# Optimization experiments

Hardware: AMD Instinct MI355X
Metric: run time of the kernel (lower is better)

## Reference

```python
import jax, jax.numpy as jnp
import numpy as np

N, M, D = 6144, 6144, 128
EPS = 1e-12


def setup_inputs() -> dict:
    key = jax.random.key(0)
    k1, k2 = jax.random.split(key)
    desc1 = jax.random.normal(k1, (N, D), dtype=jnp.float32)
    desc2 = jax.random.normal(k2, (M, D), dtype=jnp.float32)
    # DISK descriptors are unit-normalized; distances in the docstring are in [0, 2]
    desc1 = desc1 / jnp.linalg.norm(desc1, axis=-1, keepdims=True)
    desc2 = desc2 / jnp.linalg.norm(desc2, axis=-1, keepdims=True)
    inverse_T = jnp.asarray(15.0, dtype=jnp.float32)  # learned scalar nn.Parameter
    return {"desc1": desc1, "desc2": desc2, "inverse_T": inverse_T}


def reference(desc1, desc2, inverse_T):
    # pairwise Euclidean distance matrix [N, M]
    sq1 = jnp.sum(desc1 * desc1, axis=-1)            # [N]
    sq2 = jnp.sum(desc2 * desc2, axis=-1)            # [M]
    inner = desc1 @ desc2.T                           # [N, M] GEMM, D=128
    d2 = sq1[:, None] + sq2[None, :] - 2.0 * inner
    distances = jnp.sqrt(jnp.maximum(d2, 0.0) + EPS)  # [N, M]

    affinity = -inverse_T * distances                 # scaled logits

    # Categorical(logits=affinity).logits  == log_softmax over rows
    # Categorical(logits=affinity.T).logits.T == log_softmax over columns
    logp_I = jax.nn.log_softmax(affinity, axis=1)     # row distribution [N, M]
    logp_T = jax.nn.log_softmax(affinity, axis=0)     # col distribution [N, M]

    dense_logp = logp_I + logp_T                      # dual-softmax log prob
    dense_p = jnp.exp(logp_I) * jnp.exp(logp_T)       # dual-softmax prob

    # mle(): argmax matches with cycle-consistency check
    maxes_I = jnp.argmax(affinity, axis=1)            # [N] best col per row
    maxes_T = jnp.argmax(affinity, axis=0)            # [M] best row per col
    idx = jnp.arange(N)
    cycle_consistent = maxes_T[maxes_I] == idx        # [N] bool mask
    # Original returns stack([right[paired_left], paired_left]) over the
    # consistent subset; here we keep fixed shape [2, N] + the mask
    # (matches[:, i] valid iff cycle_consistent[i]).
    matches = jnp.stack([idx, maxes_I], axis=0)       # [2, N] int

    return dense_logp, dense_p, matches, cycle_consistent
```

## Files before the change

kernel.cpp:

```cpp
#include <hip/hip_runtime.h>
#include <hip/hip_bf16.h>
#include <stdint.h>

#define NROWS 6144
#define MCOLS 6144
#define DDIM  128
#define EPSQ  1e-12f
#define NTC   48

typedef unsigned long long ull;
typedef __attribute__((ext_vector_type(8))) short short8;
typedef __attribute__((ext_vector_type(4))) float floatx4;

__device__ __forceinline__ ull makeKey(float v, int idx) {
    unsigned u = __float_as_uint(v);
    u = (u & 0x80000000u) ? ~u : (u | 0x80000000u);
    return ((ull)u << 32) | (ull)(0xFFFFFFFFu - (unsigned)idx);
}
__device__ __forceinline__ int decodeKeyIdx(ull k) {
    return (int)(0xFFFFFFFFu - (unsigned)(k & 0xFFFFFFFFull));
}
__device__ __forceinline__ unsigned short f2bf(float f) {
    unsigned u = __float_as_uint(f);
    u += 0x7fffu + ((u >> 16) & 1);
    return (unsigned short)(u >> 16);
}

#define DPPF(x, ctrl) __uint_as_float(__builtin_amdgcn_update_dpp( \
    0, (int)__float_as_uint(x), (ctrl), 0xF, 0xF, false))
#define DPPI(x, ctrl) __builtin_amdgcn_update_dpp(0, (x), (ctrl), 0xF, 0xF, false)
#define ROR8 0x128
#define ROR4 0x124
#define ROR2 0x122
#define ROR1 0x121

#define GLOAD16(g, l) \
  __builtin_amdgcn_global_load_lds((const __attribute__((address_space(1))) unsigned int*)(g), \
                                   (__attribute__((address_space(3))) unsigned int*)(l), 16, 0, 0)

__device__ __forceinline__ void tileCoord(int& rowBase, int& colBase) {
    int id  = blockIdx.x;
    int wid = (id & 7) * (NTC * NTC / 8) + (id >> 3);
    rowBase = (wid / NTC) * 128;
    colBase = (wid % NTC) * 128;
}

__global__ __launch_bounds__(256) void convert_kernel(
    const float* __restrict__ d1, const float* __restrict__ d2,
    unsigned short* __restrict__ s1, unsigned short* __restrict__ s2,
    float* __restrict__ sq1, float* __restrict__ sq2,
    unsigned* __restrict__ zero_region)
{
    int tid = blockIdx.x * 256 + threadIdx.x;
    if (tid < 36864) zero_region[tid] = 0u;

    int row = tid >> 4;
    int sub = tid & 15;
    if (row >= NROWS + MCOLS) return;
    bool isA = row < NROWS;
    int r = isA ? row : row - NROWS;
    const float* src = (isA ? d1 : d2) + (size_t)r * DDIM + sub * 8;
    unsigned short* dst = (isA ? s1 : s2) + (size_t)r * 256;

    float4 v0 = *(const float4*)(src);
    float4 v1 = *(const float4*)(src + 4);
    float vs[8] = {v0.x, v0.y, v0.z, v0.w, v1.x, v1.y, v1.z, v1.w};

    float s = 0.f;
    #pragma unroll
    for (int j = 0; j < 8; ++j) s += vs[j] * vs[j];
    #pragma unroll
    for (int m = 1; m < 16; m <<= 1) s += __shfl_xor(s, m, 64);
    if (sub == 0) { if (isA) sq1[r] = s; else sq2[r] = s; }

    short8 hi, lo;
    #pragma unroll
    for (int j = 0; j < 8; ++j) {
        unsigned short h = f2bf(vs[j]);
        hi[j] = (short)h;
        lo[j] = (short)f2bf(vs[j] - __uint_as_float((unsigned)h << 16));
    }
    int e  = sub * 8;
    int c  = e >> 6;
    int pe = (e & 63) ^ ((r & 7) << 3);
    *(short8*)(dst + c * 128 + pe)      = hi;
    *(short8*)(dst + c * 128 + 64 + pe) = lo;
}

__device__ __forceinline__ void stageBuf(
    const unsigned short* __restrict__ gpanel, unsigned short* buf,
    int c, int h, int t)
{
    #pragma unroll
    for (int it = 0; it < 2; ++it) {
        int li = t * 8 + it * 4096;
        int r  = li >> 6, e = li & 63;
        int gi = r * 256 + c * 128 + h * 64 + e;
        GLOAD16(gpanel + gi, &buf[li]);
    }
}

__device__ __forceinline__ void computeSplit(
    const unsigned short* Ab_, const unsigned short* Bb_,
    int lane, int wr, int wc, floatx4 acc[4][2])
{
    const int l15 = lane & 15;
    const int q16 = (lane >> 4) * 16;
    const int sw  = (l15 & 7) << 4;
    const char* Ab = (const char*)Ab_;
    const char* Bb = (const char*)Bb_;
    #pragma unroll
    for (int ks = 0; ks < 2; ++ks) {
        const int kk = (ks * 64 + q16) ^ sw;
        short8 af[4], bf[2];
        #pragma unroll
        for (int mi = 0; mi < 4; ++mi)
            af[mi] = *(const short8*)(Ab + (wr * 64 + mi * 16 + l15) * 128 + kk);
        #pragma unroll
        for (int ni = 0; ni < 2; ++ni)
            bf[ni] = *(const short8*)(Bb + (wc * 32 + ni * 16 + l15) * 128 + kk);
        #pragma unroll
        for (int mi = 0; mi < 4; ++mi)
            #pragma unroll
            for (int ni = 0; ni < 2; ++ni)
                acc[mi][ni] = __builtin_amdgcn_mfma_f32_16x16x32_bf16(
                    bf[ni], af[mi], acc[mi][ni], 0, 0, 0);
    }
}

__device__ __forceinline__ void computeSplitAB2(
    const unsigned short* Ab_, const unsigned short* B0_, const unsigned short* B1_,
    int lane, int wr, int wc, floatx4 acc[4][2])
{
    const int l15 = lane & 15;
    const int q16 = (lane >> 4) * 16;
    const int sw  = (l15 & 7) << 4;
    const char* Ab = (const char*)Ab_;
    const char* B0 = (const char*)B0_;
    const char* B1 = (const char*)B1_;
    #pragma unroll
    for (int ks = 0; ks < 2; ++ks) {
        const int kk = (ks * 64 + q16) ^ sw;
        short8 af[4], bf0[2], bf1[2];
        #pragma unroll
        for (int mi = 0; mi < 4; ++mi)
            af[mi] = *(const short8*)(Ab + (wr * 64 + mi * 16 + l15) * 128 + kk);
        #pragma unroll
        for (int ni = 0; ni < 2; ++ni) {
            bf0[ni] = *(const short8*)(B0 + (wc * 32 + ni * 16 + l15) * 128 + kk);
            bf1[ni] = *(const short8*)(B1 + (wc * 32 + ni * 16 + l15) * 128 + kk);
        }
        #pragma unroll
        for (int mi = 0; mi < 4; ++mi)
            #pragma unroll
            for (int ni = 0; ni < 2; ++ni)
                acc[mi][ni] = __builtin_amdgcn_mfma_f32_16x16x32_bf16(
                    bf0[ni], af[mi], acc[mi][ni], 0, 0, 0);
        #pragma unroll
        for (int mi = 0; mi < 4; ++mi)
            #pragma unroll
            for (int ni = 0; ni < 2; ++ni)
                acc[mi][ni] = __builtin_amdgcn_mfma_f32_16x16x32_bf16(
                    bf1[ni], af[mi], acc[mi][ni], 0, 0, 0);
    }
}

__global__ __launch_bounds__(512, 4) void gemm_reduce_kernel(
    const unsigned short* __restrict__ s1, const unsigned short* __restrict__ s2,
    const float* __restrict__ invT,
    const float* __restrict__ sq1, const float* __restrict__ sq2,
    float* __restrict__ rowsum, float* __restrict__ colsum,
    ull* __restrict__ rowkey, ull* __restrict__ colkey)
{
    __shared__ unsigned short A0[8192], A1[8192], B0[8192], B1[8192];
    __shared__ float lRowS[128], lColS[128];
    __shared__ ull   lRowK[128], lColK[128];

    const int t = threadIdx.x;
    const int lane = t & 63;
    const int wave = t >> 6;
    const int wr = wave >> 2, wc = wave & 3;
    int rowBase, colBase;
    tileCoord(rowBase, colBase);
    const unsigned short* gA = s1 + (size_t)rowBase * 256;
    const unsigned short* gB = s2 + (size_t)colBase * 256;

    if (t < 128) { lRowS[t] = 0.f; lColS[t] = 0.f; lRowK[t] = 0ull; lColK[t] = 0ull; }

    floatx4 acc[4][2] = {};
    stageBuf(gA, A0, 0, 0, t); stageBuf(gB, B0, 0, 0, t); stageBuf(gB, B1, 0, 1, t);
    __syncthreads();
    stageBuf(gA, A1, 0, 1, t);
    computeSplitAB2(A0, B0, B1, lane, wr, wc, acc);
    __syncthreads();
    stageBuf(gA, A0, 1, 0, t); stageBuf(gB, B1, 1, 0, t);
    computeSplit(A1, B0, lane, wr, wc, acc);
    __syncthreads();
    stageBuf(gA, A1, 1, 1, t); stageBuf(gB, B0, 1, 1, t);
    computeSplit(A0, B1, lane, wr, wc, acc);
    __syncthreads();
    computeSplit(A0, B0, lane, wr, wc, acc);
    computeSplit(A1, B1, lane, wr, wc, acc);

    const int l15 = lane & 15;
    const int q   = lane >> 4;
    const float iT = *invT;
    float s1r[4];
    #pragma unroll
    for (int mi = 0; mi < 4; ++mi)
        s1r[mi] = sq1[rowBase + wr * 64 + mi * 16 + l15] + EPSQ;
    const int colLoc0 = wc * 32 + q * 4;
    float4 s2v[2];
    #pragma unroll
    for (int ni = 0; ni < 2; ++ni)
        s2v[ni] = *(const float4*)(sq2 + colBase + colLoc0 + ni * 16);

    float rs[4], rv[4]; int rj[4];
    float cs[2][4], cv[2][4]; int ci[2][4];
    #pragma unroll
    for (int ni = 0; ni < 2; ++ni)
        #pragma unroll
        for (int r = 0; r < 4; ++r) { cs[ni][r] = 0.f; cv[ni][r] = -1e30f; ci[ni][r] = 0; }

    #pragma unroll
    for (int mi = 0; mi < 4; ++mi) {
        const int gi = rowBase + wr * 64 + mi * 16 + l15;
        rs[mi] = 0.f; rv[mi] = -1e30f; rj[mi] = 0;
        #pragma unroll
        for (int ni = 0; ni < 2; ++ni) {
            #pragma unroll
            for (int r = 0; r < 4; ++r) {
                float sv2 = (r == 0) ? s2v[ni].x : (r == 1) ? s2v[ni].y
                          : (r == 2) ? s2v[ni].z : s2v[ni].w;
                float dd = s1r[mi] + sv2 - 2.0f * acc[mi][ni][r];
                float v = -iT * __builtin_amdgcn_sqrtf(fmaxf(dd, EPSQ));
                float e = __expf(v);
                rs[mi] += e;
                if (v > rv[mi]) { rv[mi] = v; rj[mi] = colBase + colLoc0 + ni * 16 + r; }
                cs[ni][r] += e;
                if (v > cv[ni][r]) { cv[ni][r] = v; ci[ni][r] = gi; }
            }
        }
    }

    #pragma unroll
    for (int mi = 0; mi < 4; ++mi) {
        float s = rs[mi];
        s += __shfl_xor(s, 16, 64); s += __shfl_xor(s, 32, 64);
        float v = rv[mi];
        v = fmaxf(v, __shfl_xor(v, 16, 64)); v = fmaxf(v, __shfl_xor(v, 32, 64));
        int cand = (rv[mi] == v) ? rj[mi] : 0x7FFFFFFF;
        cand = min(cand, __shfl_xor(cand, 16, 64));
        cand = min(cand, __shfl_xor(cand, 32, 64));
        if (lane < 16) {
            int idx = wr * 64 + mi * 16 + l15;
            atomicAdd(&lRowS[idx], s);
            atomicMax(&lRowK[idx], makeKey(v, cand));
        }
    }

    #pragma unroll
    for (int ni = 0; ni < 2; ++ni)
        #pragma unroll
        for (int r = 0; r < 4; ++r) {
            float s = cs[ni][r];
            s += DPPF(s, ROR8); s += DPPF(s, ROR4); s += DPPF(s, ROR2); s += DPPF(s, ROR1);
            float v = cv[ni][r];
            v = fmaxf(v, DPPF(v, ROR8)); v = fmaxf(v, DPPF(v, ROR4));
            v = fmaxf(v, DPPF(v, ROR2)); v = fmaxf(v, DPPF(v, ROR1));
            int cand = (cv[ni][r] == v) ? ci[ni][r] : 0x7FFFFFFF;
            cand = min(cand, DPPI(cand, ROR8)); cand = min(cand, DPPI(cand, ROR4));
            cand = min(cand, DPPI(cand, ROR2)); cand = min(cand, DPPI(cand, ROR1));
            if (l15 == 0) {
                int idx = colLoc0 + ni * 16 + r;
                atomicAdd(&lColS[idx], s);
                atomicMax(&lColK[idx], makeKey(v, cand));
            }
        }
    __syncthreads();

    if (t < 128) {
        atomicAdd(&rowsum[rowBase + t], lRowS[t]);
        atomicMax(&rowkey[rowBase + t], lRowK[t]);
    } else if (t < 256) {
        int j = t - 128;
        atomicAdd(&colsum[colBase + j], lColS[j]);
        atomicMax(&colkey[colBase + j], lColK[j]);
    }
}

#define VSTRIDE 132
__global__ __launch_bounds__(512, 4) void gemm_write_kernel(
    const unsigned short* __restrict__ s1, const unsigned short* __restrict__ s2,
    const float* __restrict__ invT,
    const float* __restrict__ sq1, const float* __restrict__ sq2,
    const float* __restrict__ rowsum, const float* __restrict__ colsum,
    const ull* __restrict__ rowkey, const ull* __restrict__ colkey,
    float* __restrict__ logp_out, float* __restrict__ p_out,
    float* __restrict__ out_matches, float* __restrict__ out_cyc)
{
    __shared__ char SMEM[128 * VSTRIDE * 4];
    unsigned short* A0 = (unsigned short*)(SMEM);
    unsigned short* A1 = (unsigned short*)(SMEM + 16384);
    unsigned short* B0 = (unsigned short*)(SMEM + 32768);
    unsigned short* B1 = (unsigned short*)(SMEM + 49152);
    float* V = (float*)SMEM;

    const int t = threadIdx.x;
    const int lane = t & 63;
    const int wave = t >> 6;
    const int wr = wave >> 2, wc = wave & 3;
    int rowBase, colBase;
    tileCoord(rowBase, colBase);
    const unsigned short* gA = s1 + (size_t)rowBase * 256;
    const unsigned short* gB = s2 + (size_t)colBase * 256;

    if (colBase == 0 && t < 128) {
        int i = rowBase + t;
        int mi = decodeKeyIdx(rowkey[i]);
        out_matches[i]         = (float)i;
        out_matches[NROWS + i] = (float)mi;
        out_cyc[i] = (decodeKeyIdx(colkey[mi]) == i) ? 1.0f : 0.0f;
    }

    floatx4 acc[4][2] = {};
    stageBuf(gA, A0, 0, 0, t); stageBuf(gB, B0, 0, 0, t);
    __syncthreads();
    stageBuf(gA, A1, 0, 1, t); stageBuf(gB, B1, 1, 0, t);
    computeSplit(A0, B0, lane, wr, wc, acc);
    __syncthreads();
    stageBuf(gA, A0, 1, 0, t);
    computeSplit(A1, B0, lane, wr, wc, acc);
    __syncthreads();
    stageBuf(gA, A1, 1, 1, t);
    computeSplit(A0, B1, lane, wr, wc, acc);
    __syncthreads();
    computeSplit(A1, B1, lane, wr, wc, acc);

    const int l15 = lane & 15;
    const int q   = lane >> 4;
    const float iT = *invT;
    float s1r[4];
    #pragma unroll
    for (int mi = 0; mi < 4; ++mi)
        s1r[mi] = sq1[rowBase + wr * 64 + mi * 16 + l15] + EPSQ;
    const int colLoc0 = wc * 32 + q * 4;
    float4 s2v[2];
    #pragma unroll
    for (int ni = 0; ni < 2; ++ni)
        s2v[ni] = *(const float4*)(sq2 + colBase + colLoc0 + ni * 16);

    __syncthreads();
    #pragma unroll
    for (int mi = 0; mi < 4; ++mi) {
        const int lrow = wr * 64 + mi * 16 + l15;
        #pragma unroll
        for (int ni = 0; ni < 2; ++ni) {
            floatx4 vv;
            #pragma unroll
            for (int r = 0; r < 4; ++r) {
                float sv2 = (r == 0) ? s2v[ni].x : (r == 1) ? s2v[ni].y
                          : (r == 2) ? s2v[ni].z : s2v[ni].w;
                float dd = s1r[mi] + sv2 - 2.0f * acc[mi][ni][r];
                vv[r] = -iT * __builtin_amdgcn_sqrtf(fmaxf(dd, EPSQ));
            }
            *(floatx4*)(V + lrow * VSTRIDE + colLoc0 + ni * 16) = vv;
        }
    }
    __syncthreads();

    const int rsub = lane >> 4;
    const int csub = (lane & 15) * 4;
    #pragma unroll
    for (int g = 0; g < 4; ++g) {
        const int lrow = wave * 16 + g * 4 + rsub;
        const int grow = rowBase + lrow;
        const float rl = logf(rowsum[grow]);
        #pragma unroll
        for (int h = 0; h < 2; ++h) {
            const int lcol = h * 64 + csub;
            float4 csum = *(const float4*)(colsum + colBase + lcol);
            float4 cl;
            cl.x = logf(csum.x); cl.y = logf(csum.y);
            cl.z = logf(csum.z); cl.w = logf(csum.w);
            float4 v4 = *(const float4*)(V + lrow * VSTRIDE + lcol);
            floatx4 ov, pv;
            ov[0] = (v4.x - rl) + (v4.x - cl.x); pv[0] = __expf(ov[0]);
            ov[1] = (v4.y - rl) + (v4.y - cl.y); pv[1] = __expf(ov[1]);
            ov[2] = (v4.z - rl) + (v4.z - cl.z); pv[2] = __expf(ov[2]);
            ov[3] = (v4.w - rl) + (v4.w - cl.w); pv[3] = __expf(ov[3]);
            size_t off = (size_t)grow * MCOLS + colBase + lcol;
            __builtin_nontemporal_store(ov, (floatx4*)(logp_out + off));
            __builtin_nontemporal_store(pv, (floatx4*)(p_out + off));
        }
    }
}

extern "C" void kernel_launch(void* const* d_in, const int* in_sizes, int n_in,
                              void* d_out, int out_size, void* d_ws, size_t ws_size,
                              hipStream_t stream) {
    const float* d1   = (const float*)d_in[0];
    const float* d2   = (const float*)d_in[1];
    const float* invT = (const float*)d_in[2];

    float* out     = (float*)d_out;
    float* logp    = out;
    float* pout    = out + (size_t)NROWS * MCOLS;
    float* matches = out + 2ull * NROWS * MCOLS;
    float* cyc     = matches + 2 * NROWS;

    char* ws = (char*)d_ws;
    float* rowsum = (float*)(ws + 0);
    float* colsum = (float*)(ws + 24576);
    ull*   rowkey = (ull*)(ws + 49152);
    ull*   colkey = (ull*)(ws + 98304);
    float* sq1    = (float*)(ws + 147456);
    float* sq2    = (float*)(ws + 172032);
    unsigned short* s1 = (unsigned short*)(ws + 270336);
    unsigned short* s2 = (unsigned short*)(ws + 270336 + 3145728);

    convert_kernel<<<(NROWS + MCOLS) * 16 / 256, 256, 0, stream>>>(
        d1, d2, s1, s2, sq1, sq2, (unsigned*)ws);

    gemm_reduce_kernel<<<NTC * NTC, 512, 0, stream>>>(
        s1, s2, invT, sq1, sq2, rowsum, colsum, rowkey, colkey);

    gemm_write_kernel<<<NTC * NTC, 512, 0, stream>>>(
        s1, s2, invT, sq1, sq2, rowsum, colsum, rowkey, colkey,
        logp, pout, matches, cyc);
}
```

Before: 127.9 us.

## Restructure split-bf16 GEMM staging into two K-chunks with fewer barriers

```diff
diff --git a/kernel.cpp b/kernel.cpp
--- a/kernel.cpp
+++ b/kernel.cpp
@@ -100,68 +100,88 @@
     }
 }
 
-__device__ __forceinline__ void computeSplit(
-    const unsigned short* Ab_, const unsigned short* Bb_,
+__device__ __forceinline__ void computeChunk3(
+    const unsigned short* Ah_, const unsigned short* Al_,
+    const unsigned short* Bh_, const unsigned short* Bl_,
     int lane, int wr, int wc, floatx4 acc[4][2])
 {
     const int l15 = lane & 15;
     const int q16 = (lane >> 4) * 16;
     const int sw  = (l15 & 7) << 4;
-    const char* Ab = (const char*)Ab_;
-    const char* Bb = (const char*)Bb_;
+    const char* Ah = (const char*)Ah_;
+    const char* Al = (const char*)Al_;
+    const char* Bh = (const char*)Bh_;
+    const char* Bl = (const char*)Bl_;
     #pragma unroll
     for (int ks = 0; ks < 2; ++ks) {
         const int kk = (ks * 64 + q16) ^ sw;
-        short8 af[4], bf[2];
-        #pragma unroll
-        for (int mi = 0; mi < 4; ++mi)
-            af[mi] = *(const short8*)(Ab + (wr * 64 + mi * 16 + l15) * 128 + kk);
-        #pragma unroll
-        for (int ni = 0; ni < 2; ++ni)
-            bf[ni] = *(const short8*)(Bb + (wc * 32 + ni * 16 + l15) * 128 + kk);
+        short8 afh[4], afl[4], bfh[2], bfl[2];
+        #pragma unroll
+        for (int mi = 0; mi < 4; ++mi) {
+            afh[mi] = *(const short8*)(Ah + (wr * 64 + mi * 16 + l15) * 128 + kk);
+            afl[mi] = *(const short8*)(Al + (wr * 64 + mi * 16 + l15) * 128 + kk);
+        }
+        #pragma unroll
+        for (int ni = 0; ni < 2; ++ni) {
+            bfh[ni] = *(const short8*)(Bh + (wc * 32 + ni * 16 + l15) * 128 + kk);
+            bfl[ni] = *(const short8*)(Bl + (wc * 32 + ni * 16 + l15) * 128 + kk);
+        }
         #pragma unroll
         for (int mi = 0; mi < 4; ++mi)
             #pragma unroll
             for (int ni = 0; ni < 2; ++ni)
                 acc[mi][ni] = __builtin_amdgcn_mfma_f32_16x16x32_bf16(
-                    bf[ni], af[mi], acc[mi][ni], 0, 0, 0);
-    }
-}
-
-__device__ __forceinline__ void computeSplitAB2(
-    const unsigned short* Ab_, const unsigned short* B0_, const unsigned short* B1_,
+                    bfh[ni], afh[mi], acc[mi][ni], 0, 0, 0);
+        #pragma unroll
+        for (int mi = 0; mi < 4; ++mi)
+            #pragma unroll
+            for (int ni = 0; ni < 2; ++ni)
+                acc[mi][ni] = __builtin_amdgcn_mfma_f32_16x16x32_bf16(
+                    bfl[ni], afh[mi], acc[mi][ni], 0, 0, 0);
+        #pragma unroll
+        for (int mi = 0; mi < 4; ++mi)
+            #pragma unroll
+            for (int ni = 0; ni < 2; ++ni)
+                acc[mi][ni] = __builtin_amdgcn_mfma_f32_16x16x32_bf16(
+                    bfh[ni], afl[mi], acc[mi][ni], 0, 0, 0);
+    }
+}
+
+__device__ __forceinline__ void computeChunk2(
+    const unsigned short* Ah_, const unsigned short* Al_,
+    const unsigned short* Bh_,
     int lane, int wr, int wc, floatx4 acc[4][2])
 {
     const int l15 = lane & 15;
     const int q16 = (lane >> 4) * 16;
     const int sw  = (l15 & 7) << 4;
-    const char* Ab = (const char*)Ab_;
-    const char* B0 = (const char*)B0_;
-    const char* B1 = (const char*)B1_;
+    const char* Ah = (const char*)Ah_;
+    const char* Al = (const char*)Al_;
+    const char* Bh = (const char*)Bh_;
     #pragma unroll
     for (int ks = 0; ks < 2; ++ks) {
         const int kk = (ks * 64 + q16) ^ sw;
-        short8 af[4], bf0[2], bf1[2];
-        #pragma unroll
-        for (int mi = 0; mi < 4; ++mi)
-            af[mi] = *(const short8*)(Ab + (wr * 64 + mi * 16 + l15) * 128 + kk);
-        #pragma unroll
-        for (int ni = 0; ni < 2; ++ni) {
-            bf0[ni] = *(const short8*)(B0 + (wc * 32 + ni * 16 + l15) * 128 + kk);
-            bf1[ni] = *(const short8*)(B1 + (wc * 32 + ni * 16 + l15) * 128 + kk);
-        }
+        short8 afh[4], afl[4], bfh[2];
+        #pragma unroll
+        for (int mi = 0; mi < 4; ++mi) {
+            afh[mi] = *(const short8*)(Ah + (wr * 64 + mi * 16 + l15) * 128 + kk);
+            afl[mi] = *(const short8*)(Al + (wr * 64 + mi * 16 + l15) * 128 + kk);
+        }
+        #pragma unroll
+        for (int ni = 0; ni < 2; ++ni)
+            bfh[ni] = *(const short8*)(Bh + (wc * 32 + ni * 16 + l15) * 128 + kk);
         #pragma unroll
         for (int mi = 0; mi < 4; ++mi)
             #pragma unroll
             for (int ni = 0; ni < 2; ++ni)
                 acc[mi][ni] = __builtin_amdgcn_mfma_f32_16x16x32_bf16(
-                    bf0[ni], af[mi], acc[mi][ni], 0, 0, 0);
+                    bfh[ni], afh[mi], acc[mi][ni], 0, 0, 0);
         #pragma unroll
         for (int mi = 0; mi < 4; ++mi)
             #pragma unroll
             for (int ni = 0; ni < 2; ++ni)
                 acc[mi][ni] = __builtin_amdgcn_mfma_f32_16x16x32_bf16(
-                    bf1[ni], af[mi], acc[mi][ni], 0, 0, 0);
+                    bfh[ni], afl[mi], acc[mi][ni], 0, 0, 0);
     }
 }
 
@@ -188,19 +208,15 @@
     if (t < 128) { lRowS[t] = 0.f; lColS[t] = 0.f; lRowK[t] = 0ull; lColK[t] = 0ull; }
 
     floatx4 acc[4][2] = {};
-    stageBuf(gA, A0, 0, 0, t); stageBuf(gB, B0, 0, 0, t); stageBuf(gB, B1, 0, 1, t);
-    __syncthreads();
-    stageBuf(gA, A1, 0, 1, t);
-    computeSplitAB2(A0, B0, B1, lane, wr, wc, acc);
-    __syncthreads();
-    stageBuf(gA, A0, 1, 0, t); stageBuf(gB, B1, 1, 0, t);
-    computeSplit(A1, B0, lane, wr, wc, acc);
-    __syncthreads();
-    stageBuf(gA, A1, 1, 1, t); stageBuf(gB, B0, 1, 1, t);
-    computeSplit(A0, B1, lane, wr, wc, acc);
-    __syncthreads();
-    computeSplit(A0, B0, lane, wr, wc, acc);
-    computeSplit(A1, B1, lane, wr, wc, acc);
+    stageBuf(gA, A0, 0, 0, t); stageBuf(gA, A1, 0, 1, t);
+    stageBuf(gB, B0, 0, 0, t); stageBuf(gB, B1, 0, 1, t);
+    __syncthreads();
+    computeChunk3(A0, A1, B0, B1, lane, wr, wc, acc);
+    __syncthreads();
+    stageBuf(gA, A0, 1, 0, t); stageBuf(gA, A1, 1, 1, t);
+    stageBuf(gB, B0, 1, 0, t); stageBuf(gB, B1, 1, 1, t);
+    __syncthreads();
+    computeChunk3(A0, A1, B0, B1, lane, wr, wc, acc);
 
     const int l15 = lane & 15;
     const int q   = lane >> 4;
@@ -324,18 +340,14 @@
     }
 
     floatx4 acc[4][2] = {};
-    stageBuf(gA, A0, 0, 0, t); stageBuf(gB, B0, 0, 0, t);
-    __syncthreads();
-    stageBuf(gA, A1, 0, 1, t); stageBuf(gB, B1, 1, 0, t);
-    computeSplit(A0, B0, lane, wr, wc, acc);
-    __syncthreads();
-    stageBuf(gA, A0, 1, 0, t);
-    computeSplit(A1, B0, lane, wr, wc, acc);
-    __syncthreads();
-    stageBuf(gA, A1, 1, 1, t);
-    computeSplit(A0, B1, lane, wr, wc, acc);
-    __syncthreads();
-    computeSplit(A1, B1, lane, wr, wc, acc);
+    stageBuf(gA, A0, 0, 0, t); stageBuf(gA, A1, 0, 1, t);
+    stageBuf(gB, B0, 0, 0, t); stageBuf(gB, B1, 1, 0, t);
+    __syncthreads();
+    computeChunk2(A0, A1, B0, lane, wr, wc, acc);
+    __syncthreads();
+    stageBuf(gA, A0, 1, 0, t); stageBuf(gA, A1, 1, 1, t);
+    __syncthreads();
+    computeChunk2(A0, A1, B1, lane, wr, wc, acc);
 
     const int l15 = lane & 15;
     const int q   = lane >> 4;
```

Measured after the change: 128.9 us. No clear change (+0.8%).
